# Optimization experiments

Measured on AMD Instinct MI355X. Metric: run time of the kernel, lower is better.

The kernel has to match this reference:

```python
import jax, jax.numpy as jnp
import numpy as np

LEVELS = ((64, 176), (32, 88), (16, 44), (8, 22))
S_TOTAL = sum(h * w for h, w in LEVELS)  # 14960
C = 128; HH = 8; HD = 16; R = 4; L = 4; P = 8
G = 32; PC_MIN = -4.0; PC_MAX = 4.0
NUM_CLASSES = 17; PROP = 3 + 3 + 4 + 1 + NUM_CLASSES  # 28


def _ln(x, g, b):
    m = x.mean(-1, keepdims=True)
    v = ((x - m) ** 2).mean(-1, keepdims=True)
    return (x - m) * jax.lax.rsqrt(v + 1e-5) * g + b


def setup_inputs() -> dict:
    key = jax.random.key(0)
    ks = jax.random.split(key, 20)
    B, N, CAM = 1, 1024, 6
    d = {}
    d['query'] = jax.random.normal(ks[0], (B, N, C), jnp.float32)
    d['gaussian_props'] = jax.random.normal(ks[1], (B, N, PROP), jnp.float32)
    d['ms_feats'] = jax.random.normal(ks[2], (B, CAM, S_TOTAL, C), jnp.float32)
    d['depth_maps'] = jax.random.uniform(ks[3], (B, CAM, 64, 176), jnp.float32, 0.5, 50.0)
    d['lidar2img'] = jax.random.normal(ks[4], (B, CAM, 4, 4), jnp.float32)
    d['img_h'] = 256
    d['img_w'] = 704
    w = lambda k, shp: jax.random.normal(k, shp, jnp.float32) * 0.02
    d['W_sc'] = w(ks[5], (3, 3, 3, C, C)); d['b_sc'] = jnp.zeros((C,), jnp.float32)
    d['sc_g'] = jnp.ones((C,), jnp.float32); d['sc_b'] = jnp.zeros((C,), jnp.float32)
    d['ref_off_w'] = w(ks[6], (C, R * 3)); d['ref_off_b'] = jnp.zeros((R * 3,), jnp.float32)
    d['off_w'] = w(ks[7], (C, HH * R * L * P * 2)); d['off_b'] = jnp.zeros((HH * R * L * P * 2,), jnp.float32)
    d['aw_w'] = w(ks[8], (C, HH * R * L * P)); d['aw_b'] = jnp.zeros((HH * R * L * P,), jnp.float32)
    d['val_w'] = w(ks[9], (C, C)); d['val_b'] = jnp.zeros((C,), jnp.float32)
    d['out_w'] = w(ks[10], (C, C)); d['out_b'] = jnp.zeros((C,), jnp.float32)
    d['an_g'] = jnp.ones((C,), jnp.float32); d['an_b'] = jnp.zeros((C,), jnp.float32)
    d['f1_w'] = w(ks[11], (C, 4 * C)); d['f1_b'] = jnp.zeros((4 * C,), jnp.float32)
    d['f2_w'] = w(ks[12], (4 * C, C)); d['f2_b'] = jnp.zeros((C,), jnp.float32)
    d['fn_g'] = jnp.ones((C,), jnp.float32); d['fn_b'] = jnp.zeros((C,), jnp.float32)
    d['p1_w'] = w(ks[13], (C, C)); d['p1_b'] = jnp.zeros((C,), jnp.float32)
    d['p2_w'] = w(ks[14], (C, PROP)); d['p2_b'] = jnp.zeros((PROP,), jnp.float32)
    return d


def _forward(query, gaussian_props, ms_feats, depth_maps, lidar2img,
             W_sc, b_sc, sc_g, sc_b, ref_off_w, ref_off_b, off_w, off_b,
             aw_w, aw_b, val_w, val_b, out_w, out_b, an_g, an_b,
             f1_w, f1_b, f2_w, f2_b, fn_g, fn_b, p1_w, p1_b, p2_w, p2_b,
             img_h, img_w):
    B, N, _ = query.shape
    CAM = ms_feats.shape[1]
    means = gaussian_props[..., :3]
    # ---- SparseConv3DBlock: scatter-mean voxelization, 3x3x3 conv, gather back ----
    vs = (PC_MAX - PC_MIN) / G
    vox = jnp.clip(jnp.floor((means - PC_MIN) / vs).astype(jnp.int32), 0, G - 1)
    flat = (vox[..., 0] * G + vox[..., 1]) * G + vox[..., 2]  # [B,N]
    bi = jnp.arange(B)[:, None]
    grid = jnp.zeros((B, G * G * G, C), query.dtype).at[bi, flat].add(query)
    cnt = jnp.zeros((B, G * G * G, 1), query.dtype).at[bi, flat].add(1.0)
    grid = (grid / jnp.maximum(cnt, 1.0)).reshape(B, G, G, G, C)
    grid = jax.lax.conv_general_dilated(grid, W_sc, (1, 1, 1), 'SAME',
                                        dimension_numbers=('NDHWC', 'DHWIO', 'NDHWC')) + b_sc
    grid = jax.nn.gelu(grid).reshape(B, G * G * G, C)
    query = _ln(query + grid[bi, flat], sc_g, sc_b)
    # ---- DeformableAttention3D ----
    fW = jnp.asarray(img_w, query.dtype); fH = jnp.asarray(img_h, query.dtype)
    ref3d = means[:, :, None, :] + (query @ ref_off_w + ref_off_b).reshape(B, N, R, 3)
    pts = jnp.concatenate([ref3d, jnp.ones_like(ref3d[..., :1])], -1)
    proj = jnp.einsum('bcij,bnrj->bcnri', lidar2img, pts)  # [B,CAM,N,R,4]
    z = proj[..., 2]; zc = jnp.maximum(z, 1e-5)
    u = proj[..., 0] / zc; v = proj[..., 1] / zc
    valid = (z > 1e-5) & (u >= 0) & (u < fW) & (v >= 0) & (v < fH)
    Hd, Wd = depth_maps.shape[2], depth_maps.shape[3]
    iu = jnp.clip((u / fW * Wd).astype(jnp.int32), 0, Wd - 1)
    iv = jnp.clip((v / fH * Hd).astype(jnp.int32), 0, Hd - 1)
    ds = jnp.take_along_axis(depth_maps.reshape(B, CAM, Hd * Wd),
                             (iv * Wd + iu).reshape(B, CAM, N * R), axis=2).reshape(B, CAM, N, R)
    wmask = jnp.exp(-jnp.abs(z - ds)) * valid.astype(query.dtype)  # [B,CAM,N,R]
    ref2 = jnp.stack([u / fW, v / fH], -1)  # [B,CAM,N,R,2]
    offs = (query @ off_w + off_b).reshape(B, N, HH, R, L, P, 2)
    attn = jax.nn.softmax((query @ aw_w + aw_b).reshape(B, N, HH, R * L * P), -1)
    attn = attn.reshape(B, N, HH, R, L, P)
    value = (ms_feats @ val_w + val_b).reshape(B, CAM, S_TOTAL, HH, HD)
    out = jnp.zeros((B, N, HH, HD), query.dtype)
    s0 = 0
    for l, (Hl, Wl) in enumerate(LEVELS):
        sz = Hl * Wl
        vl = value[:, :, s0:s0 + sz].transpose(0, 1, 3, 2, 4).reshape(B * CAM, HH, sz, HD)
        s0 += sz
        off_l = offs[:, :, :, :, l]  # [B,N,HH,R,P,2]
        loc = ref2[:, :, :, None, :, None, :] + off_l[:, None] / jnp.array([Wl, Hl], query.dtype)
        # loc: [B,CAM,N,HH,R,P,2] in normalized coords
        x = (loc[..., 0] * Wl - 0.5).transpose(0, 1, 3, 2, 4, 5).reshape(B * CAM, HH, N * R * P)
        y = (loc[..., 1] * Hl - 0.5).transpose(0, 1, 3, 2, 4, 5).reshape(B * CAM, HH, N * R * P)
        x0 = jnp.floor(x); y0 = jnp.floor(y); wx = x - x0; wy = y - y0
        x0i = jnp.clip(x0.astype(jnp.int32), 0, Wl - 1)
        x1i = jnp.clip(x0.astype(jnp.int32) + 1, 0, Wl - 1)
        y0i = jnp.clip(y0.astype(jnp.int32), 0, Hl - 1)
        y1i = jnp.clip(y0.astype(jnp.int32) + 1, 0, Hl - 1)
        g = lambda ix, iy: jnp.take_along_axis(vl, (iy * Wl + ix)[..., None], axis=2)
        samp = (((1 - wx) * (1 - wy))[..., None] * g(x0i, y0i)
                + (wx * (1 - wy))[..., None] * g(x1i, y0i)
                + ((1 - wx) * wy)[..., None] * g(x0i, y1i)
                + (wx * wy)[..., None] * g(x1i, y1i))  # [B*CAM,HH,N*R*P,HD]
        samp = samp.reshape(B, CAM, HH, N, R, P, HD)
        ws = attn[:, :, :, :, l, :][:, None].transpose(0, 1, 3, 2, 4, 5) * wmask[:, :, None, :, :, None]
        out = out + jnp.einsum('bchnrp,bchnrpd->bnhd', ws, samp)
    attn_out = out.reshape(B, N, C) @ out_w + out_b
    query = _ln(query + attn_out, an_g, an_b)
    query = _ln(query + (jax.nn.gelu(query @ f1_w + f1_b) @ f2_w + f2_b), fn_g, fn_b)
    props = gaussian_props + (jax.nn.gelu(query @ p1_w + p1_b) @ p2_w + p2_b)
    return query, props


def reference(query, gaussian_props, ms_feats, depth_maps, lidar2img,
              W_sc, b_sc, sc_g, sc_b, ref_off_w, ref_off_b, off_w, off_b,
              aw_w, aw_b, val_w, val_b, out_w, out_b, an_g, an_b,
              f1_w, f1_b, f2_w, f2_b, fn_g, fn_b, p1_w, p1_b, p2_w, p2_b,
              img_h, img_w):
    return _forward(query, gaussian_props, ms_feats, depth_maps, lidar2img,
                    W_sc, b_sc, sc_g, sc_b, ref_off_w, ref_off_b, off_w, off_b,
                    aw_w, aw_b, val_w, val_b, out_w, out_b, an_g, an_b,
                    f1_w, f1_b, f2_w, f2_b, fn_g, fn_b, p1_w, p1_b, p2_w, p2_b,
                    img_h, img_w)
```

## Files before the change

kernel.cpp:

```cpp
#include <hip/hip_runtime.h>
#include <hip/hip_bf16.h>
#include <math.h>

#define NQ    1024
#define CC    128
#define CAM   6
#define RR    4
#define LL    4
#define PP    8
#define HHD   8
#define HDD   16
#define GG    32
#define S_TOT 14960
#define PROPN 28
#define NTAP  27
#define MVAL  (CAM * S_TOT)
#define NVB   ((MVAL + 63) / 64)

typedef __attribute__((ext_vector_type(8))) short bf16x8;
typedef __attribute__((ext_vector_type(4))) float f32x4;

__device__ __forceinline__ float gelu_tanh(float x) {
    return 0.5f * x * (1.0f + tanhf(0.7978845608028654f * (x + 0.044715f * x * x * x)));
}

__device__ __forceinline__ unsigned short f2bf(float f) {
    union { float f; unsigned int u; } x; x.f = f;
    unsigned int r = (x.u + 0x7FFFu + ((x.u >> 16) & 1u)) >> 16;
    return (unsigned short)r;
}

__device__ __forceinline__ float bf2f(short s) {
    union { unsigned int u; float f; } x;
    x.u = ((unsigned int)(unsigned short)s) << 16;
    return x.f;
}

__global__ void k_wt_scatter(const float* __restrict__ Wsc, unsigned short* __restrict__ WscT,
                             const float* __restrict__ valw, unsigned short* __restrict__ valwT,
                             const float* __restrict__ outw, unsigned short* __restrict__ outwT,
                             const float* __restrict__ p1w, unsigned short* __restrict__ p1wT,
                             const float* __restrict__ f1w, unsigned short* __restrict__ f1wT,
                             const float* __restrict__ f2w, unsigned short* __restrict__ f2wT,
                             const float* __restrict__ offw, unsigned short* __restrict__ offwT,
                             const float* __restrict__ aww, unsigned short* __restrict__ awwT,
                             const float* __restrict__ p2w, unsigned short* __restrict__ p2wT,
                             const float* __restrict__ p2b, float* __restrict__ p2bp,
                             const float* __restrict__ qin, const float* __restrict__ gp,
                             float* __restrict__ grid, float* __restrict__ cnt,
                             int* __restrict__ flatidx) {
    __shared__ float t[64][65];
    __shared__ int sflat[2];
    int z = blockIdx.z;
    int tid = threadIdx.x;

    if (z >= 63) {
        int half = tid >> 7, c = tid & 127;
        int n = ((z - 63) * 4 + (blockIdx.x * 2 + blockIdx.y)) * 2 + half;
        if (c == 0) {
            float mx = gp[n * PROPN + 0], my = gp[n * PROPN + 1], mz = gp[n * PROPN + 2];
            int vx = (int)floorf((mx + 4.0f) * 4.0f);
            int vy = (int)floorf((my + 4.0f) * 4.0f);
            int vz = (int)floorf((mz + 4.0f) * 4.0f);
            vx = min(max(vx, 0), GG - 1);
            vy = min(max(vy, 0), GG - 1);
            vz = min(max(vz, 0), GG - 1);
            int f = (vx * GG + vy) * GG + vz;
            sflat[half] = f;
            flatidx[n] = f;
            atomicAdd(&cnt[f], 1.0f);
        }
        __syncthreads();
        atomicAdd(&grid[(size_t)sflat[half] * CC + c], qin[(size_t)n * CC + c]);
        return;
    }

    int n0 = blockIdx.x * 64, k0 = blockIdx.y * 64;
    if (z == 62) {
#pragma unroll
        for (int it = 0; it < 16; ++it) {
            int idx = tid + it * 256;
            int r = idx >> 6, c = idx & 63;
            t[r][c] = (n0 + c < PROPN) ? p2w[(size_t)(k0 + r) * PROPN + n0 + c] : 0.f;
        }
        __syncthreads();
#pragma unroll
        for (int it = 0; it < 16; ++it) {
            int idx = tid + it * 256;
            int r = idx >> 6, c = idx & 63;
            p2wT[(size_t)(n0 + r) * 128 + k0 + c] = f2bf(t[c][r]);
        }
        if (blockIdx.x == 0 && blockIdx.y == 0 && tid < 128)
            p2bp[tid] = (tid < PROPN) ? p2b[tid] : 0.f;
        return;
    }
    const float* src; unsigned short* dst; int ss, ds;
    if (z < 27)       { src = Wsc + (size_t)z * 16384; dst = WscT + (size_t)z * 16384; ss = 128; ds = 128; }
    else if (z == 27) { src = valw; dst = valwT; ss = 128; ds = 128; }
    else if (z == 28) { src = outw; dst = outwT; ss = 128; ds = 128; }
    else if (z == 29) { src = p1w;  dst = p1wT;  ss = 128; ds = 128; }
    else if (z < 34)  { int q = z - 30; src = f1w + q * 128; dst = f1wT + (size_t)q * 16384; ss = 512;  ds = 128; }
    else if (z < 38)  { int q = z - 34; src = f2w + (size_t)q * 16384; dst = f2wT + q * 128; ss = 128;  ds = 512; }
    else if (z < 54)  { int q = z - 38; src = offw + q * 128; dst = offwT + (size_t)q * 16384; ss = 2048; ds = 128; }
    else              { int q = z - 54; src = aww + q * 128;  dst = awwT + (size_t)q * 16384; ss = 1024; ds = 128; }
#pragma unroll
    for (int it = 0; it < 16; ++it) {
        int idx = tid + it * 256;
        int r = idx >> 6, c = idx & 63;
        t[r][c] = src[(size_t)(k0 + r) * ss + n0 + c];
    }
    __syncthreads();
#pragma unroll
    for (int it = 0; it < 16; ++it) {
        int idx = tid + it * 256;
        int r = idx >> 6, c = idx & 63;
        dst[(size_t)(n0 + r) * ds + k0 + c] = f2bf(t[c][r]);
    }
}

__global__ __launch_bounds__(256) void k_conv1m(
    const float* __restrict__ grid, const float* __restrict__ cnt,
    const int* __restrict__ flatidx, const unsigned short* __restrict__ WT,
    float* __restrict__ convacc27) {
    __shared__ bf16x8 As[128 * 16];
    __shared__ bf16x8 Bs[128 * 16];
    __shared__ int   nbase[128];
    __shared__ float nscale[128];
    int tid = threadIdx.x;
    int tap = blockIdx.y;
    int q0 = blockIdx.x * 128;
    int dz = tap / 9 - 1, dy = (tap / 3) % 3 - 1, dx = tap % 3 - 1;

    if (tid < 128) {
        int f = flatidx[q0 + tid];
        int nx = (f >> 10) + dz, ny = ((f >> 5) & 31) + dy, nz = (f & 31) + dx;
        bool ok = (nx >= 0 && nx < GG && ny >= 0 && ny < GG && nz >= 0 && nz < GG);
        int nf = ok ? (nx * GG + ny) * GG + nz : 0;
        nbase[tid] = nf;
        nscale[tid] = ok ? 1.0f / fmaxf(cnt[nf], 1.0f) : 0.f;
    }
    __syncthreads();
#pragma unroll
    for (int it = 0; it < 8; ++it) {
        int idx = tid + it * 256;
        int m = idx >> 4, c = idx & 15;
        const float* p = grid + (size_t)nbase[m] * CC + c * 8;
        float s = nscale[m];
        float4 a = *(const float4*)p;
        float4 b = *(const float4*)(p + 4);
        bf16x8 u;
        u[0] = (short)f2bf(a.x * s); u[1] = (short)f2bf(a.y * s);
        u[2] = (short)f2bf(a.z * s); u[3] = (short)f2bf(a.w * s);
        u[4] = (short)f2bf(b.x * s); u[5] = (short)f2bf(b.y * s);
        u[6] = (short)f2bf(b.z * s); u[7] = (short)f2bf(b.w * s);
        As[m * 16 + (c ^ (m & 15))] = u;
    }
    const unsigned short* Wt = WT + (size_t)tap * CC * CC;
#pragma unroll
    for (int it = 0; it < 8; ++it) {
        int idx = tid + it * 256;
        int n = idx >> 4, c = idx & 15;
        bf16x8 w = *(const bf16x8*)(Wt + (size_t)n * CC + c * 8);
        Bs[n * 16 + (c ^ (n & 15))] = w;
    }
    __syncthreads();

    int lane = tid & 63, wv = tid >> 6;
    int wr = (wv >> 1) * 64, wc = (wv & 1) * 64;
    int r = lane & 15, q = lane >> 4;
    f32x4 acc[4][4];
#pragma unroll
    for (int i = 0; i < 4; ++i)
#pragma unroll
        for (int j = 0; j < 4; ++j)
#pragma unroll
            for (int e = 0; e < 4; ++e) acc[i][j][e] = 0.f;
#pragma unroll
    for (int ks = 0; ks < 4; ++ks) {
        bf16x8 bfr[4];
#pragma unroll
        for (int j = 0; j < 4; ++j)
            bfr[j] = Bs[(wc + j * 16 + r) * 16 + ((ks * 4 + q) ^ r)];
#pragma unroll
        for (int i = 0; i < 4; ++i) {
            bf16x8 af = As[(wr + i * 16 + r) * 16 + ((ks * 4 + q) ^ r)];
#pragma unroll
            for (int j = 0; j < 4; ++j)
                acc[i][j] = __builtin_amdgcn_mfma_f32_16x16x32_bf16(af, bfr[j], acc[i][j], 0, 0, 0);
        }
    }
    float* dst = convacc27 + (size_t)tap * NQ * CC;
#pragma unroll
    for (int i = 0; i < 4; ++i)
#pragma unroll
        for (int e = 0; e < 4; ++e) {
            int m = q0 + wr + i * 16 + q * 4 + e;
#pragma unroll
            for (int j = 0; j < 4; ++j) {
                int col = wc + j * 16 + r;
                dst[(size_t)m * CC + col] = acc[i][j][e];
            }
        }
}

__global__ void k_ln_conv_proj(const float* __restrict__ a, const float* __restrict__ convacc27,
                               const float* __restrict__ bconv,
                               const float* __restrict__ g, const float* __restrict__ be,
                               float* __restrict__ out, unsigned short* __restrict__ outbf,
                               const float* __restrict__ refw, const float* __restrict__ refb,
                               const float* __restrict__ gp, const float* __restrict__ l2i,
                               const float* __restrict__ depth,
                               const int* __restrict__ ih, const int* __restrict__ iw,
                               float* __restrict__ wm, float* __restrict__ r2u,
                               float* __restrict__ r2v) {
    int n = blockIdx.x, c = threadIdx.x;
    float apart = 0.f;
#pragma unroll
    for (int t = 0; t < NTAP; ++t) apart += convacc27[((size_t)t * NQ + n) * CC + c];
    float x = a[n * CC + c] + gelu_tanh(apart + bconv[c]);
    __shared__ float w4[4];
    __shared__ float qrow[CC];
    __shared__ float ro[12];
    float s = x;
#pragma unroll
    for (int d = 1; d < 64; d <<= 1) s += __shfl_xor(s, d);
    if ((c & 63) == 0) w4[c >> 6] = s;
    __syncthreads();
    float m = (w4[0] + w4[1]) * (1.0f / CC);
    float dd = x - m;
    float v = dd * dd;
#pragma unroll
    for (int d = 1; d < 64; d <<= 1) v += __shfl_xor(v, d);
    if ((c & 63) == 0) w4[2 + (c >> 6)] = v;
    __syncthreads();
    float var = (w4[2] + w4[3]) * (1.0f / CC);
    float qv = dd * rsqrtf(var + 1e-5f) * g[c] + be[c];
    out[n * CC + c] = qv;
    outbf[n * CC + c] = f2bf(qv);
    qrow[c] = qv;
    __syncthreads();
    if (c < 12) {
        float sacc = refb[c];
#pragma unroll 4
        for (int k = 0; k < 128; ++k) sacc += qrow[k] * refw[k * 12 + c];
        ro[c] = sacc;
    }
    __syncthreads();
    if (c < 24) {
        int cam = c >> 2, r = c & 3;
        float fH = (float)(*ih), fW = (float)(*iw);
        const float* M = l2i + cam * 16;
        float px = gp[n * PROPN + 0] + ro[r * 3 + 0];
        float py = gp[n * PROPN + 1] + ro[r * 3 + 1];
        float pz = gp[n * PROPN + 2] + ro[r * 3 + 2];
        float p0 = M[0] * px + M[1] * py + M[2]  * pz + M[3];
        float p1 = M[4] * px + M[5] * py + M[6]  * pz + M[7];
        float p2 = M[8] * px + M[9] * py + M[10] * pz + M[11];
        float zc = fmaxf(p2, 1e-5f);
        float u = p0 / zc, vv = p1 / zc;
        bool valid = (p2 > 1e-5f) && (u >= 0.f) && (u < fW) && (vv >= 0.f) && (vv < fH);
        int iu = min(max((int)(u / fW * 176.f), 0), 175);
        int iv = min(max((int)(vv / fH * 64.f), 0), 63);
        float ds = depth[cam * 64 * 176 + iv * 176 + iu];
        int o = cam * (NQ * RR) + n * RR + r;
        wm[o]  = valid ? expf(-fabsf(p2 - ds)) : 0.f;
        r2u[o] = u / fW;
        r2v[o] = vv / fH;
    }
}

union QVSm {
    bf16x8 Bs[128 * 16];
    struct { bf16x8 Bs[128 * 16]; unsigned short Os[64 * 128]; float sbias[128]; } v;
};
__global__ __launch_bounds__(256) void k_qhead_val(
    const unsigned short* __restrict__ Abf,
    const unsigned short* __restrict__ offwT, const float* __restrict__ offb,
    unsigned short* __restrict__ offsb,
    const unsigned short* __restrict__ awwT, const float* __restrict__ awb,
    unsigned short* __restrict__ attn,
    const float* __restrict__ ms, const unsigned short* __restrict__ valwT,
    const float* __restrict__ valb, unsigned short* __restrict__ value)
{
    __shared__ QVSm sm;
    int bx = blockIdx.x, tid = threadIdx.x;
    int lane = tid & 63, wv = tid >> 6;
    int r = lane & 15, q = lane >> 4;

    if (bx >= 24) {
        int vb = (bx - 24) * 8 + blockIdx.y;
        if (vb >= NVB) return;
        int m0 = vb * 64;
#pragma unroll
        for (int it = 0; it < 8; ++it) {
            int idx = tid + it * 256;
            int n = idx >> 4, c = idx & 15;
            sm.v.Bs[n * 16 + (c ^ (n & 15))] = *(const bf16x8*)(valwT + (size_t)n * 128 + c * 8);
        }
        if (tid < 128) sm.v.sbias[tid] = valb[tid];
        __syncthreads();

        int row = m0 + wv * 16 + r;
        int mg = min(row, MVAL - 1);
        const float* pA = ms + (size_t)mg * 128;

        f32x4 acc[8];
#pragma unroll
        for (int j = 0; j < 8; ++j)
#pragma unroll
            for (int e = 0; e < 4; ++e) acc[j][e] = 0.f;

#pragma unroll
        for (int ks = 0; ks < 4; ++ks) {
            const float* p = pA + ks * 32 + q * 8;
            float4 a = *(const float4*)p;
            float4 b = *(const float4*)(p + 4);
            bf16x8 af;
            af[0] = (short)f2bf(a.x); af[1] = (short)f2bf(a.y);
            af[2] = (short)f2bf(a.z); af[3] = (short)f2bf(a.w);
            af[4] = (short)f2bf(b.x); af[5] = (short)f2bf(b.y);
            af[6] = (short)f2bf(b.z); af[7] = (short)f2bf(b.w);
            bf16x8 bfr[8];
#pragma unroll
            for (int j = 0; j < 8; ++j)
                bfr[j] = sm.v.Bs[(j * 16 + r) * 16 + ((ks * 4 + q) ^ r)];
#pragma unroll
            for (int j = 0; j < 8; ++j)
                acc[j] = __builtin_amdgcn_mfma_f32_16x16x32_bf16(af, bfr[j], acc[j], 0, 0, 0);
        }

#pragma unroll
        for (int j = 0; j < 8; ++j)
#pragma unroll
            for (int e = 0; e < 4; ++e) {
                int rl = wv * 16 + q * 4 + e;
                sm.v.Os[rl * 128 + j * 16 + r] = f2bf(acc[j][e] + sm.v.sbias[j * 16 + r]);
            }
        __syncthreads();
#pragma unroll
        for (int it = 0; it < 2; ++it) {
            int idx = tid + it * 256;
            int rl = idx & 63, h = idx >> 6;
            int m = m0 + rl;
            if (m < MVAL) {
                int cam = m / S_TOT;
                int s = m - cam * S_TOT;
                int pos, HW, sb;
                if (s < 11264)      { pos = s;          HW = 11264; sb = 0; }
                else if (s < 14080) { pos = s - 11264;  HW = 2816;  sb = 11264; }
                else if (s < 14784) { pos = s - 14080;  HW = 704;   sb = 14080; }
                else                { pos = s - 14784;  HW = 176;   sb = 14784; }
                size_t dst = ((size_t)cam * S_TOT + sb) * CC
                           + (size_t)h * (HW * HDD) + (size_t)pos * HDD;
                *(bf16x8*)(value + dst)     = *(const bf16x8*)&sm.v.Os[rl * 128 + h * 16];
                *(bf16x8*)(value + dst + 8) = *(const bf16x8*)&sm.v.Os[rl * 128 + h * 16 + 8];
            }
        }
        return;
    }

    bool isoff = bx < 16;
    int n0 = (isoff ? bx : (bx - 16)) * 128;
    const unsigned short* WT = isoff ? offwT : awwT;
    int m0 = blockIdx.y * 128;
    int mw = m0 + wv * 32;

#pragma unroll
    for (int it = 0; it < 8; ++it) {
        int idx = tid + it * 256;
        int n = idx >> 4, c = idx & 15;
        sm.Bs[n * 16 + (c ^ (n & 15))] = *(const bf16x8*)(WT + (size_t)(n0 + n) * 128 + c * 8);
    }
    __syncthreads();

    f32x4 acc[2][8];
#pragma unroll
    for (int i = 0; i < 2; ++i)
#pragma unroll
        for (int j = 0; j < 8; ++j)
#pragma unroll
            for (int e = 0; e < 4; ++e) acc[i][j][e] = 0.f;

#pragma unroll
    for (int ks = 0; ks < 4; ++ks) {
        bf16x8 af[2];
#pragma unroll
        for (int i = 0; i < 2; ++i)
            af[i] = *(const bf16x8*)(Abf + (size_t)(mw + i * 16 + r) * 128 + (ks * 4 + q) * 8);
#pragma unroll
        for (int j = 0; j < 8; ++j) {
            bf16x8 b = sm.Bs[(j * 16 + r) * 16 + ((ks * 4 + q) ^ r)];
#pragma unroll
            for (int i = 0; i < 2; ++i)
                acc[i][j] = __builtin_amdgcn_mfma_f32_16x16x32_bf16(af[i], b, acc[i][j], 0, 0, 0);
        }
    }

    float bia[8];
    const float* bsrc = isoff ? offb : awb;
#pragma unroll
    for (int j = 0; j < 8; ++j) bia[j] = bsrc[n0 + j * 16 + r];

    if (isoff) {
#pragma unroll
        for (int i = 0; i < 2; ++i)
#pragma unroll
            for (int e = 0; e < 4; ++e) {
                int m = mw + i * 16 + q * 4 + e;
                unsigned short* orow = offsb + (size_t)m * 2048 + n0;
#pragma unroll
                for (int j = 0; j < 8; ++j)
                    orow[j * 16 + r] = f2bf(acc[i][j][e] + bia[j]);
            }
    } else {
#pragma unroll
        for (int i = 0; i < 2; ++i)
#pragma unroll
            for (int e = 0; e < 4; ++e) {
                float mx = -1e30f;
#pragma unroll
                for (int j = 0; j < 8; ++j) mx = fmaxf(mx, acc[i][j][e] + bia[j]);
#pragma unroll
                for (int d = 1; d < 16; d <<= 1) mx = fmaxf(mx, __shfl_xor(mx, d));
                float ex[8];
                float sum = 0.f;
#pragma unroll
                for (int j = 0; j < 8; ++j) { ex[j] = expf(acc[i][j][e] + bia[j] - mx); sum += ex[j]; }
#pragma unroll
                for (int d = 1; d < 16; d <<= 1) sum += __shfl_xor(sum, d);
                float inv = 1.0f / sum;
                int m = mw + i * 16 + q * 4 + e;
                unsigned short* orow = attn + (size_t)m * 1024 + n0;
#pragma unroll
                for (int j = 0; j < 8; ++j)
                    orow[j * 16 + r] = f2bf(ex[j] * inv);
            }
    }
}

__global__ __launch_bounds__(512) void k_sample(
                         const unsigned short* __restrict__ value,
                         const unsigned short* __restrict__ offsb,
                         const unsigned short* __restrict__ attn,
                         const float* __restrict__ wm,
// ... 311 lines not shown
        int m = m0 + q * 4 + e;
        int cl = wc + r;
        if (cl < PROPN)
            outp[(size_t)m * PROPN + cl] = acc[e] + p2bp[cl] + gp[(size_t)m * PROPN + cl];
    }
}

extern "C" void kernel_launch(void* const* d_in, const int* in_sizes, int n_in,
                              void* d_out, int out_size, void* d_ws, size_t ws_size,
                              hipStream_t stream) {
    const float* query = (const float*)d_in[0];
    const float* gp    = (const float*)d_in[1];
    const float* ms    = (const float*)d_in[2];
    const float* depth = (const float*)d_in[3];
    const float* l2i   = (const float*)d_in[4];
    const int*   ih    = (const int*)d_in[5];
    const int*   iw    = (const int*)d_in[6];
    const float* Wsc   = (const float*)d_in[7];
    const float* bsc   = (const float*)d_in[8];
    const float* scg   = (const float*)d_in[9];
    const float* scb   = (const float*)d_in[10];
    const float* refw  = (const float*)d_in[11];
    const float* refb  = (const float*)d_in[12];
    const float* offw  = (const float*)d_in[13];
    const float* offbi = (const float*)d_in[14];
    const float* aww   = (const float*)d_in[15];
    const float* awb   = (const float*)d_in[16];
    const float* valw  = (const float*)d_in[17];
    const float* valb  = (const float*)d_in[18];
    const float* outw  = (const float*)d_in[19];
    const float* outb  = (const float*)d_in[20];
    const float* ang   = (const float*)d_in[21];
    const float* anb   = (const float*)d_in[22];
    const float* f1w   = (const float*)d_in[23];
    const float* f1b   = (const float*)d_in[24];
    const float* f2w   = (const float*)d_in[25];
    const float* f2b   = (const float*)d_in[26];
    const float* fng   = (const float*)d_in[27];
    const float* fnb   = (const float*)d_in[28];
    const float* p1w   = (const float*)d_in[29];
    const float* p1b   = (const float*)d_in[30];
    const float* p2w   = (const float*)d_in[31];
    const float* p2b   = (const float*)d_in[32];

    float* outq = (float*)d_out;
    float* outp = outq + NQ * CC;

    float* ws = (float*)d_ws;
    size_t o = 0;
    float* grid    = ws + o; o += (size_t)GG * GG * GG * CC;
    float* cnt     = ws + o; o += GG * GG * GG;
    size_t zero_floats = o;
    int*   flatidx = (int*)(ws + o); o += NQ;
    float* convacc27 = ws + o; o += (size_t)NTAP * NQ * CC;
    float* q1      = ws + o; o += NQ * CC;
    float* wm      = ws + o; o += CAM * NQ * RR;
    float* r2u     = ws + o; o += CAM * NQ * RR;
    float* r2v     = ws + o; o += CAM * NQ * RR;
    float* sampout = ws + o; o += NQ * CC;
    float* p2bp    = ws + o; o += 128;
    unsigned short* u16base = (unsigned short*)(ws + o);
    size_t uo = 0;
    unsigned short* value = u16base + uo; uo += (size_t)CAM * S_TOT * CC;
    unsigned short* offsb = u16base + uo; uo += (size_t)NQ * 2048;
    unsigned short* attn  = u16base + uo; uo += (size_t)NQ * 1024;
    unsigned short* q1bf  = u16base + uo; uo += (size_t)NQ * CC;
    unsigned short* offwT = u16base + uo; uo += (size_t)2048 * 128;
    unsigned short* awwT  = u16base + uo; uo += (size_t)1024 * 128;
    unsigned short* valwT = u16base + uo; uo += 128 * 128;
    unsigned short* outwT = u16base + uo; uo += 128 * 128;
    unsigned short* f1wT  = u16base + uo; uo += 512 * 128;
    unsigned short* f2wT  = u16base + uo; uo += 128 * 512;
    unsigned short* p1wT  = u16base + uo; uo += 128 * 128;
    unsigned short* p2wT  = u16base + uo; uo += 128 * 128;
    unsigned short* WscT  = u16base + uo; uo += (size_t)27 * 128 * 128;
    (void)ws_size; (void)in_sizes; (void)n_in; (void)out_size;

    hipMemsetAsync(ws, 0, zero_floats * sizeof(float), stream);

    k_wt_scatter<<<dim3(2, 2, 63 + 128), 256, 0, stream>>>(
        Wsc, WscT, valw, valwT, outw, outwT, p1w, p1wT, f1w, f1wT, f2w, f2wT,
        offw, offwT, aww, awwT, p2w, p2wT, p2b, p2bp,
        query, gp, grid, cnt, flatidx);

    k_conv1m<<<dim3(8, 27), 256, 0, stream>>>(grid, cnt, flatidx, WscT, convacc27);
    k_ln_conv_proj<<<NQ, CC, 0, stream>>>(query, convacc27, bsc, scg, scb, q1, q1bf,
                                          refw, refb, gp, l2i, depth, ih, iw, wm, r2u, r2v);

    k_qhead_val<<<dim3(24 + 176, 8), 256, 0, stream>>>(
        q1bf, offwT, offbi, offsb, awwT, awb, attn,
        ms, valwT, valb, value);

    k_sample<<<NQ, 512, 0, stream>>>(value, offsb, attn, wm, r2u, r2v, sampout);

    k_tail<<<64, 512, 0, stream>>>(sampout, outwT, outb, q1, ang, anb,
                                   f1wT, f1b, f2wT, f2b, fng, fnb,
                                   p1wT, p1b, p2wT, p2bp, gp, outq, outp);
}
```

Before: 221.5 us.

## Fuse sparse-conv tap loop with LayerNorm/projection and co-schedule with value projection

The 27-tap sparse conv now accumulates all taps in registers within one block per 128 queries, instead of writing 27 partial tiles to global memory and reducing them in a separate kernel. The GELU, LayerNorm, reference-offset projection and camera projection run in the same kernel epilogue. That kernel also hosts the value-projection blocks, so the value GEMM overlaps with the serial conv blocks. The query-head GEMM becomes its own launch. This removes the large convacc27 buffer traffic and one launch, but only 8 blocks now handle the conv, each looping serially over 27 taps, which limits parallelism on that path.

```diff
diff --git a/kernel.cpp b/kernel.cpp
--- a/kernel.cpp
+++ b/kernel.cpp
@@ -34,6 +34,15 @@
     union { unsigned int u; float f; } x;
     x.u = ((unsigned int)(unsigned short)s) << 16;
     return x.f;
+}
+
+__device__ __forceinline__ void nbns_calc(int f, int tap, const float* __restrict__ cnt,
+                                          int& nfo, float& nso) {
+    int dz = tap / 9 - 1, dy = (tap / 3) % 3 - 1, dx = tap % 3 - 1;
+    int nx = (f >> 10) + dz, ny = ((f >> 5) & 31) + dy, nz = (f & 31) + dx;
+    bool ok = (nx >= 0 && nx < GG && ny >= 0 && ny < GG && nz >= 0 && nz < GG);
+    nfo = ok ? (nx * GG + ny) * GG + nz : 0;
+    nso = ok ? 1.0f / fmaxf(cnt[nfo], 1.0f) : 0.f;
 }
 
 __global__ void k_wt_scatter(const float* __restrict__ Wsc, unsigned short* __restrict__ WscT,
@@ -118,178 +127,35 @@
     }
 }
 
-__global__ __launch_bounds__(256) void k_conv1m(
+union CLSm {
+    struct { bf16x8 As[128 * 16]; bf16x8 Bs[128 * 16]; } c;
+    float xrow[128 * 128];
+    struct { bf16x8 Bs[128 * 16]; unsigned short Os[64 * 128]; float sbias[128]; } v;
+};
+__global__ __launch_bounds__(256) void k_conv_ln_val(
     const float* __restrict__ grid, const float* __restrict__ cnt,
     const int* __restrict__ flatidx, const unsigned short* __restrict__ WT,
-    float* __restrict__ convacc27) {
-    __shared__ bf16x8 As[128 * 16];
-    __shared__ bf16x8 Bs[128 * 16];
-    __shared__ int   nbase[128];
-    __shared__ float nscale[128];
-    int tid = threadIdx.x;
-    int tap = blockIdx.y;
-    int q0 = blockIdx.x * 128;
-    int dz = tap / 9 - 1, dy = (tap / 3) % 3 - 1, dx = tap % 3 - 1;
-
-    if (tid < 128) {
-        int f = flatidx[q0 + tid];
-        int nx = (f >> 10) + dz, ny = ((f >> 5) & 31) + dy, nz = (f & 31) + dx;
-        bool ok = (nx >= 0 && nx < GG && ny >= 0 && ny < GG && nz >= 0 && nz < GG);
-        int nf = ok ? (nx * GG + ny) * GG + nz : 0;
-        nbase[tid] = nf;
-        nscale[tid] = ok ? 1.0f / fmaxf(cnt[nf], 1.0f) : 0.f;
-    }
-    __syncthreads();
-#pragma unroll
-    for (int it = 0; it < 8; ++it) {
-        int idx = tid + it * 256;
-        int m = idx >> 4, c = idx & 15;
-        const float* p = grid + (size_t)nbase[m] * CC + c * 8;
-        float s = nscale[m];
-        float4 a = *(const float4*)p;
-        float4 b = *(const float4*)(p + 4);
-        bf16x8 u;
-        u[0] = (short)f2bf(a.x * s); u[1] = (short)f2bf(a.y * s);
-        u[2] = (short)f2bf(a.z * s); u[3] = (short)f2bf(a.w * s);
-        u[4] = (short)f2bf(b.x * s); u[5] = (short)f2bf(b.y * s);
-        u[6] = (short)f2bf(b.z * s); u[7] = (short)f2bf(b.w * s);
-        As[m * 16 + (c ^ (m & 15))] = u;
-    }
-    const unsigned short* Wt = WT + (size_t)tap * CC * CC;
-#pragma unroll
-    for (int it = 0; it < 8; ++it) {
-        int idx = tid + it * 256;
-        int n = idx >> 4, c = idx & 15;
-        bf16x8 w = *(const bf16x8*)(Wt + (size_t)n * CC + c * 8);
-        Bs[n * 16 + (c ^ (n & 15))] = w;
-    }
-    __syncthreads();
-
-    int lane = tid & 63, wv = tid >> 6;
-    int wr = (wv >> 1) * 64, wc = (wv & 1) * 64;
-    int r = lane & 15, q = lane >> 4;
-    f32x4 acc[4][4];
-#pragma unroll
-    for (int i = 0; i < 4; ++i)
-#pragma unroll
-        for (int j = 0; j < 4; ++j)
-#pragma unroll
-            for (int e = 0; e < 4; ++e) acc[i][j][e] = 0.f;
-#pragma unroll
-    for (int ks = 0; ks < 4; ++ks) {
-        bf16x8 bfr[4];
-#pragma unroll
-        for (int j = 0; j < 4; ++j)
-            bfr[j] = Bs[(wc + j * 16 + r) * 16 + ((ks * 4 + q) ^ r)];
-#pragma unroll
-        for (int i = 0; i < 4; ++i) {
-            bf16x8 af = As[(wr + i * 16 + r) * 16 + ((ks * 4 + q) ^ r)];
-#pragma unroll
-            for (int j = 0; j < 4; ++j)
-                acc[i][j] = __builtin_amdgcn_mfma_f32_16x16x32_bf16(af, bfr[j], acc[i][j], 0, 0, 0);
-        }
-    }
-    float* dst = convacc27 + (size_t)tap * NQ * CC;
-#pragma unroll
-    for (int i = 0; i < 4; ++i)
-#pragma unroll
-        for (int e = 0; e < 4; ++e) {
-            int m = q0 + wr + i * 16 + q * 4 + e;
-#pragma unroll
-            for (int j = 0; j < 4; ++j) {
-                int col = wc + j * 16 + r;
-                dst[(size_t)m * CC + col] = acc[i][j][e];
-            }
-        }
-}
-
-__global__ void k_ln_conv_proj(const float* __restrict__ a, const float* __restrict__ convacc27,
-                               const float* __restrict__ bconv,
-                               const float* __restrict__ g, const float* __restrict__ be,
-                               float* __restrict__ out, unsigned short* __restrict__ outbf,
-                               const float* __restrict__ refw, const float* __restrict__ refb,
-                               const float* __restrict__ gp, const float* __restrict__ l2i,
-                               const float* __restrict__ depth,
-                               const int* __restrict__ ih, const int* __restrict__ iw,
-                               float* __restrict__ wm, float* __restrict__ r2u,
-                               float* __restrict__ r2v) {
-    int n = blockIdx.x, c = threadIdx.x;
-    float apart = 0.f;
-#pragma unroll
-    for (int t = 0; t < NTAP; ++t) apart += convacc27[((size_t)t * NQ + n) * CC + c];
-    float x = a[n * CC + c] + gelu_tanh(apart + bconv[c]);
-    __shared__ float w4[4];
-    __shared__ float qrow[CC];
-    __shared__ float ro[12];
-    float s = x;
-#pragma unroll
-    for (int d = 1; d < 64; d <<= 1) s += __shfl_xor(s, d);
-    if ((c & 63) == 0) w4[c >> 6] = s;
-    __syncthreads();
-    float m = (w4[0] + w4[1]) * (1.0f / CC);
-    float dd = x - m;
-    float v = dd * dd;
-#pragma unroll
-    for (int d = 1; d < 64; d <<= 1) v += __shfl_xor(v, d);
-    if ((c & 63) == 0) w4[2 + (c >> 6)] = v;
-    __syncthreads();
-    float var = (w4[2] + w4[3]) * (1.0f / CC);
-    float qv = dd * rsqrtf(var + 1e-5f) * g[c] + be[c];
-    out[n * CC + c] = qv;
-    outbf[n * CC + c] = f2bf(qv);
-    qrow[c] = qv;
-    __syncthreads();
-    if (c < 12) {
-        float sacc = refb[c];
-#pragma unroll 4
-        for (int k = 0; k < 128; ++k) sacc += qrow[k] * refw[k * 12 + c];
-        ro[c] = sacc;
-    }
-    __syncthreads();
-    if (c < 24) {
-        int cam = c >> 2, r = c & 3;
-        float fH = (float)(*ih), fW = (float)(*iw);
-        const float* M = l2i + cam * 16;
-        float px = gp[n * PROPN + 0] + ro[r * 3 + 0];
-        float py = gp[n * PROPN + 1] + ro[r * 3 + 1];
-        float pz = gp[n * PROPN + 2] + ro[r * 3 + 2];
-        float p0 = M[0] * px + M[1] * py + M[2]  * pz + M[3];
-        float p1 = M[4] * px + M[5] * py + M[6]  * pz + M[7];
-        float p2 = M[8] * px + M[9] * py + M[10] * pz + M[11];
-        float zc = fmaxf(p2, 1e-5f);
-        float u = p0 / zc, vv = p1 / zc;
-        bool valid = (p2 > 1e-5f) && (u >= 0.f) && (u < fW) && (vv >= 0.f) && (vv < fH);
-        int iu = min(max((int)(u / fW * 176.f), 0), 175);
-        int iv = min(max((int)(vv / fH * 64.f), 0), 63);
-        float ds = depth[cam * 64 * 176 + iv * 176 + iu];
-        int o = cam * (NQ * RR) + n * RR + r;
-        wm[o]  = valid ? expf(-fabsf(p2 - ds)) : 0.f;
-        r2u[o] = u / fW;
-        r2v[o] = vv / fH;
-    }
-}
-
-union QVSm {
-    bf16x8 Bs[128 * 16];
-    struct { bf16x8 Bs[128 * 16]; unsigned short Os[64 * 128]; float sbias[128]; } v;
-};
-__global__ __launch_bounds__(256) void k_qhead_val(
-    const unsigned short* __restrict__ Abf,
-    const unsigned short* __restrict__ offwT, const float* __restrict__ offb,
-    unsigned short* __restrict__ offsb,
-    const unsigned short* __restrict__ awwT, const float* __restrict__ awb,
-    unsigned short* __restrict__ attn,
+    const float* __restrict__ a, const float* __restrict__ bconv,
+    const float* __restrict__ g, const float* __restrict__ be,
+    float* __restrict__ q1, unsigned short* __restrict__ q1bf,
+    const float* __restrict__ refw, const float* __restrict__ refb,
+    const float* __restrict__ gp, const float* __restrict__ l2i,
+    const float* __restrict__ depth,
+    const int* __restrict__ ih, const int* __restrict__ iw,
+    float* __restrict__ wm, float* __restrict__ r2u, float* __restrict__ r2v,
     const float* __restrict__ ms, const unsigned short* __restrict__ valwT,
     const float* __restrict__ valb, unsigned short* __restrict__ value)
 {
-    __shared__ QVSm sm;
+    __shared__ CLSm sm;
+    __shared__ int   nb[128];
+    __shared__ float ns[128];
+    __shared__ float roAll[128 * 12];
     int bx = blockIdx.x, tid = threadIdx.x;
     int lane = tid & 63, wv = tid >> 6;
     int r = lane & 15, q = lane >> 4;
 
-    if (bx >= 24) {
-        int vb = (bx - 24) * 8 + blockIdx.y;
-        if (vb >= NVB) return;
+    if (bx >= 8) {
+        int vb = bx - 8;
         int m0 = vb * 64;
 #pragma unroll
         for (int it = 0; it < 8; ++it) {
@@ -313,13 +179,13 @@
 #pragma unroll
         for (int ks = 0; ks < 4; ++ks) {
             const float* p = pA + ks * 32 + q * 8;
-            float4 a = *(const float4*)p;
-            float4 b = *(const float4*)(p + 4);
+            float4 aa = *(const float4*)p;
+            float4 bb = *(const float4*)(p + 4);
             bf16x8 af;
-            af[0] = (short)f2bf(a.x); af[1] = (short)f2bf(a.y);
-            af[2] = (short)f2bf(a.z); af[3] = (short)f2bf(a.w);
-            af[4] = (short)f2bf(b.x); af[5] = (short)f2bf(b.y);
-            af[6] = (short)f2bf(b.z); af[7] = (short)f2bf(b.w);
+            af[0] = (short)f2bf(aa.x); af[1] = (short)f2bf(aa.y);
+            af[2] = (short)f2bf(aa.z); af[3] = (short)f2bf(aa.w);
+            af[4] = (short)f2bf(bb.x); af[5] = (short)f2bf(bb.y);
+            af[6] = (short)f2bf(bb.z); af[7] = (short)f2bf(bb.w);
             bf16x8 bfr[8];
 #pragma unroll
             for (int j = 0; j < 8; ++j)
@@ -359,6 +225,163 @@
         return;
     }
 
+    int q0 = bx * 128;
+    int wr = (wv >> 1) * 64, wc = (wv & 1) * 64;
+    int myflat = (tid < 128) ? flatidx[q0 + tid] : 0;
+    if (tid < 128) {
+        int nfo; float nso;
+        nbns_calc(myflat, 0, cnt, nfo, nso);
+        nb[tid] = nfo; ns[tid] = nso;
+    }
+    __syncthreads();
+
+    f32x4 acc[4][4];
+#pragma unroll
+    for (int i = 0; i < 4; ++i)
+#pragma unroll
+        for (int j = 0; j < 4; ++j)
+#pragma unroll
+            for (int e = 0; e < 4; ++e) acc[i][j][e] = 0.f;
+
+    for (int tap = 0; tap < NTAP; ++tap) {
+#pragma unroll
+        for (int it = 0; it < 8; ++it) {
+            int idx = tid + it * 256;
+            int m = idx >> 4, c = idx & 15;
+            const float* p = grid + (size_t)nb[m] * CC + c * 8;
+            float s = ns[m];
+            float4 aa = *(const float4*)p;
+            float4 bb = *(const float4*)(p + 4);
+            bf16x8 u;
+            u[0] = (short)f2bf(aa.x * s); u[1] = (short)f2bf(aa.y * s);
+            u[2] = (short)f2bf(aa.z * s); u[3] = (short)f2bf(aa.w * s);
+            u[4] = (short)f2bf(bb.x * s); u[5] = (short)f2bf(bb.y * s);
+            u[6] = (short)f2bf(bb.z * s); u[7] = (short)f2bf(bb.w * s);
+            sm.c.As[m * 16 + (c ^ (m & 15))] = u;
+        }
+        const unsigned short* Wt = WT + (size_t)tap * CC * CC;
+#pragma unroll
+        for (int it = 0; it < 8; ++it) {
+            int idx = tid + it * 256;
+            int n = idx >> 4, c = idx & 15;
+            sm.c.Bs[n * 16 + (c ^ (n & 15))] = *(const bf16x8*)(Wt + (size_t)n * CC + c * 8);
+        }
+        __syncthreads();
+        if (tid < 128 && tap < NTAP - 1) {
+            int nfo; float nso;
+            nbns_calc(myflat, tap + 1, cnt, nfo, nso);
+            nb[tid] = nfo; ns[tid] = nso;
+        }
+#pragma unroll
+        for (int ks = 0; ks < 4; ++ks) {
+            bf16x8 bfr[4];
+#pragma unroll
+            for (int j = 0; j < 4; ++j)
+                bfr[j] = sm.c.Bs[(wc + j * 16 + r) * 16 + ((ks * 4 + q) ^ r)];
+#pragma unroll
+            for (int i = 0; i < 4; ++i) {
+                bf16x8 af = sm.c.As[(wr + i * 16 + r) * 16 + ((ks * 4 + q) ^ r)];
+#pragma unroll
+                for (int j = 0; j < 4; ++j)
+                    acc[i][j] = __builtin_amdgcn_mfma_f32_16x16x32_bf16(af, bfr[j], acc[i][j], 0, 0, 0);
+            }
+        }
+        __syncthreads();
+    }
+
+#pragma unroll
+    for (int i = 0; i < 4; ++i)
+#pragma unroll
+        for (int e = 0; e < 4; ++e) {
+            int row = wr + i * 16 + q * 4 + e;
+            int n = q0 + row;
+#pragma unroll
+            for (int j = 0; j < 4; ++j) {
+                int col = wc + j * 16 + r;
+                float x = a[(size_t)n * CC + col] + gelu_tanh(acc[i][j][e] + bconv[col]);
+                sm.xrow[row * 128 + col] = x;
+            }
+        }
+    __syncthreads();
+
+    {
+        float g0 = g[lane], g1 = g[lane + 64];
+        float b0 = be[lane], b1 = be[lane + 64];
+        for (int i = 0; i < 32; ++i) {
+            int row = wv * 32 + i;
+            float x0 = sm.xrow[row * 128 + lane];
+            float x1 = sm.xrow[row * 128 + lane + 64];
+            float s = x0 + x1;
+#pragma unroll
+            for (int d = 1; d < 64; d <<= 1) s += __shfl_xor(s, d);
+            float mean = s * (1.0f / 128.0f);
+            float d0 = x0 - mean, d1 = x1 - mean;
+            float v = d0 * d0 + d1 * d1;
+#pragma unroll
+            for (int d = 1; d < 64; d <<= 1) v += __shfl_xor(v, d);
+            float rstd = rsqrtf(v * (1.0f / 128.0f) + 1e-5f);
+            float qv0 = d0 * rstd * g0 + b0;
+            float qv1 = d1 * rstd * g1 + b1;
+            int n = q0 + row;
+            q1[(size_t)n * CC + lane]      = qv0;
+            q1[(size_t)n * CC + lane + 64] = qv1;
+            q1bf[(size_t)n * CC + lane]      = f2bf(qv0);
+            q1bf[(size_t)n * CC + lane + 64] = f2bf(qv1);
+            sm.xrow[row * 128 + lane]      = qv0;
+            sm.xrow[row * 128 + lane + 64] = qv1;
+        }
+    }
+    __syncthreads();
+
+#pragma unroll
+    for (int j = 0; j < 6; ++j) {
+        int d = tid + j * 256;
+        int qq = d / 12, cc = d - qq * 12;
+        float sacc = refb[cc];
+#pragma unroll 4
+        for (int k = 0; k < 128; ++k) sacc += sm.xrow[qq * 128 + k] * refw[k * 12 + cc];
+        roAll[qq * 12 + cc] = sacc;
+    }
+    __syncthreads();
+
+    float fH = (float)(*ih), fW = (float)(*iw);
+#pragma unroll
+    for (int j = 0; j < 12; ++j) {
+        int item = tid + j * 256;
+        int nl = item / 24, c24 = item - nl * 24;
+        int cam = c24 >> 2, rr = c24 & 3;
+        const float* M = l2i + cam * 16;
+        int n = q0 + nl;
+        float px = gp[n * PROPN + 0] + roAll[nl * 12 + rr * 3 + 0];
+        float py = gp[n * PROPN + 1] + roAll[nl * 12 + rr * 3 + 1];
+        float pz = gp[n * PROPN + 2] + roAll[nl * 12 + rr * 3 + 2];
+        float p0 = M[0] * px + M[1] * py + M[2]  * pz + M[3];
+        float p1 = M[4] * px + M[5] * py + M[6]  * pz + M[7];
+        float p2 = M[8] * px + M[9] * py + M[10] * pz + M[11];
+        float zc = fmaxf(p2, 1e-5f);
+        float u = p0 / zc, vv = p1 / zc;
+        bool valid = (p2 > 1e-5f) && (u >= 0.f) && (u < fW) && (vv >= 0.f) && (vv < fH);
+        int iu = min(max((int)(u / fW * 176.f), 0), 175);
+        int iv = min(max((int)(vv / fH * 64.f), 0), 63);
+        float ds = depth[cam * 64 * 176 + iv * 176 + iu];
+        int o = cam * (NQ * RR) + n * RR + rr;
+        wm[o]  = valid ? expf(-fabsf(p2 - ds)) : 0.f;
+        r2u[o] = u / fW;
+        r2v[o] = vv / fH;
+    }
+}
+
+__global__ __launch_bounds__(256) void k_qhead(
+    const unsigned short* __restrict__ Abf,
+    const unsigned short* __restrict__ offwT, const float* __restrict__ offb,
+    unsigned short* __restrict__ offsb,
+    const unsigned short* __restrict__ awwT, const float* __restrict__ awb,
+    unsigned short* __restrict__ attn)
+{
+    __shared__ bf16x8 Bs[128 * 16];
+    int bx = blockIdx.x, tid = threadIdx.x;
+    int lane = tid & 63, wv = tid >> 6;
+    int r = lane & 15, q = lane >> 4;
     bool isoff = bx < 16;
     int n0 = (isoff ? bx : (bx - 16)) * 128;
     const unsigned short* WT = isoff ? offwT : awwT;
@@ -369,7 +392,7 @@
     for (int it = 0; it < 8; ++it) {
         int idx = tid + it * 256;
         int n = idx >> 4, c = idx & 15;
-        sm.Bs[n * 16 + (c ^ (n & 15))] = *(const bf16x8*)(WT + (size_t)(n0 + n) * 128 + c * 8);
+        Bs[n * 16 + (c ^ (n & 15))] = *(const bf16x8*)(WT + (size_t)(n0 + n) * 128 + c * 8);
     }
     __syncthreads();
 
@@ -389,7 +412,7 @@
             af[i] = *(const bf16x8*)(Abf + (size_t)(mw + i * 16 + r) * 128 + (ks * 4 + q) * 8);
 #pragma unroll
         for (int j = 0; j < 8; ++j) {
-            bf16x8 b = sm.Bs[(j * 16 + r) * 16 + ((ks * 4 + q) ^ r)];
+            bf16x8 b = Bs[(j * 16 + r) * 16 + ((ks * 4 + q) ^ r)];
 #pragma unroll
             for (int i = 0; i < 2; ++i)
                 acc[i][j] = __builtin_amdgcn_mfma_f32_16x16x32_bf16(af[i], b, acc[i][j], 0, 0, 0);
@@ -807,7 +830,6 @@
     float* cnt     = ws + o; o += GG * GG * GG;
     size_t zero_floats = o;
     int*   flatidx = (int*)(ws + o); o += NQ;
-    float* convacc27 = ws + o; o += (size_t)NTAP * NQ * CC;
     float* q1      = ws + o; o += NQ * CC;
     float* wm      = ws + o; o += CAM * NQ * RR;
     float* r2u     = ws + o; o += CAM * NQ * RR;
@@ -838,13 +860,13 @@
         offw, offwT, aww, awwT, p2w, p2wT, p2b, p2bp,
         query, gp, grid, cnt, flatidx);
 
-    k_conv1m<<<dim3(8, 27), 256, 0, stream>>>(grid, cnt, flatidx, WscT, convacc27);
-    k_ln_conv_proj<<<NQ, CC, 0, stream>>>(query, convacc27, bsc, scg, scb, q1, q1bf,
-                                          refw, refb, gp, l2i, depth, ih, iw, wm, r2u, r2v);
-
-    k_qhead_val<<<dim3(24 + 176, 8), 256, 0, stream>>>(
-        q1bf, offwT, offbi, offsb, awwT, awb, attn,
+    k_conv_ln_val<<<dim3(8 + NVB), 256, 0, stream>>>(
+        grid, cnt, flatidx, WscT,
+        query, bsc, scg, scb, q1, q1bf,
+        refw, refb, gp, l2i, depth, ih, iw, wm, r2u, r2v,
         ms, valwT, valb, value);
+
+    k_qhead<<<dim3(24, 8), 256, 0, stream>>>(q1bf, offwT, offbi, offsb, awwT, awb, attn);
 
     k_sample<<<NQ, 512, 0, stream>>>(value, offsb, attn, wm, r2u, r2v, sampout);
 
```

Measured after the change: 494.0 us. 123% more time.

## Move value projection into the conv kernel launch to overlap with conv

Applied to the files above, without the earlier changes.

The value projection blocks (ms_feats times val_w, scattered into a per-head layout) move out of the query-head kernel and into the submanifold conv kernel as extra blocks of the same grid. This lets the large, bandwidth-bound value GEMM run alongside the small 27-tap conv, which on its own launches only 216 blocks. The query-head kernel then only computes offsets and attention weights. The shared-memory union grows to cover both the conv A/B tiles and the value staging buffers, which may lower occupancy for the value blocks.

```diff
diff --git a/kernel.cpp b/kernel.cpp
--- a/kernel.cpp
+++ b/kernel.cpp
@@ -16,6 +16,7 @@
 #define NTAP  27
 #define MVAL  (CAM * S_TOT)
 #define NVB   ((MVAL + 63) / 64)
+#define NCVB  (8 * NTAP)
 
 typedef __attribute__((ext_vector_type(8))) short bf16x8;
 typedef __attribute__((ext_vector_type(4))) float f32x4;
@@ -118,17 +119,97 @@
     }
 }
 
-__global__ __launch_bounds__(256) void k_conv1m(
+union CVSm {
+    struct { bf16x8 As[128 * 16]; bf16x8 Bs[128 * 16]; } c;
+    struct { bf16x8 Bs[128 * 16]; unsigned short Os[64 * 128]; float sbias[128]; } v;
+};
+__global__ __launch_bounds__(256) void k_conv_val(
     const float* __restrict__ grid, const float* __restrict__ cnt,
     const int* __restrict__ flatidx, const unsigned short* __restrict__ WT,
-    float* __restrict__ convacc27) {
-    __shared__ bf16x8 As[128 * 16];
-    __shared__ bf16x8 Bs[128 * 16];
+    float* __restrict__ convacc27,
+    const float* __restrict__ ms, const unsigned short* __restrict__ valwT,
+    const float* __restrict__ valb, unsigned short* __restrict__ value)
+{
+    __shared__ CVSm sm;
     __shared__ int   nbase[128];
     __shared__ float nscale[128];
-    int tid = threadIdx.x;
-    int tap = blockIdx.y;
-    int q0 = blockIdx.x * 128;
+    int bx = blockIdx.x, tid = threadIdx.x;
+    int lane = tid & 63, wv = tid >> 6;
+    int r = lane & 15, q = lane >> 4;
+
+    if (bx >= NCVB) {
+        int vb = bx - NCVB;
+        int m0 = vb * 64;
+#pragma unroll
+        for (int it = 0; it < 8; ++it) {
+            int idx = tid + it * 256;
+            int n = idx >> 4, c = idx & 15;
+            sm.v.Bs[n * 16 + (c ^ (n & 15))] = *(const bf16x8*)(valwT + (size_t)n * 128 + c * 8);
+        }
+        if (tid < 128) sm.v.sbias[tid] = valb[tid];
+        __syncthreads();
+
+        int row = m0 + wv * 16 + r;
+        int mg = min(row, MVAL - 1);
+        const float* pA = ms + (size_t)mg * 128;
+
+        f32x4 acc[8];
+#pragma unroll
+        for (int j = 0; j < 8; ++j)
+#pragma unroll
+            for (int e = 0; e < 4; ++e) acc[j][e] = 0.f;
+
+#pragma unroll
+        for (int ks = 0; ks < 4; ++ks) {
+            const float* p = pA + ks * 32 + q * 8;
+            float4 aa = *(const float4*)p;
+            float4 bb = *(const float4*)(p + 4);
+            bf16x8 af;
+            af[0] = (short)f2bf(aa.x); af[1] = (short)f2bf(aa.y);
+            af[2] = (short)f2bf(aa.z); af[3] = (short)f2bf(aa.w);
+            af[4] = (short)f2bf(bb.x); af[5] = (short)f2bf(bb.y);
+            af[6] = (short)f2bf(bb.z); af[7] = (short)f2bf(bb.w);
+            bf16x8 bfr[8];
+#pragma unroll
+            for (int j = 0; j < 8; ++j)
+                bfr[j] = sm.v.Bs[(j * 16 + r) * 16 + ((ks * 4 + q) ^ r)];
+#pragma unroll
+            for (int j = 0; j < 8; ++j)
+                acc[j] = __builtin_amdgcn_mfma_f32_16x16x32_bf16(af, bfr[j], acc[j], 0, 0, 0);
+        }
+
+#pragma unroll
+        for (int j = 0; j < 8; ++j)
+#pragma unroll
+            for (int e = 0; e < 4; ++e) {
+                int rl = wv * 16 + q * 4 + e;
+                sm.v.Os[rl * 128 + j * 16 + r] = f2bf(acc[j][e] + sm.v.sbias[j * 16 + r]);
+            }
+        __syncthreads();
+#pragma unroll
+        for (int it = 0; it < 2; ++it) {
+            int idx = tid + it * 256;
+            int rl = idx & 63, h = idx >> 6;
+            int m = m0 + rl;
+            if (m < MVAL) {
+                int cam = m / S_TOT;
+                int s = m - cam * S_TOT;
+                int pos, HW, sb;
+                if (s < 11264)      { pos = s;          HW = 11264; sb = 0; }
+                else if (s < 14080) { pos = s - 11264;  HW = 2816;  sb = 11264; }
+                else if (s < 14784) { pos = s - 14080;  HW = 704;   sb = 14080; }
+                else                { pos = s - 14784;  HW = 176;   sb = 14784; }
+                size_t dst = ((size_t)cam * S_TOT + sb) * CC
+                           + (size_t)h * (HW * HDD) + (size_t)pos * HDD;
+                *(bf16x8*)(value + dst)     = *(const bf16x8*)&sm.v.Os[rl * 128 + h * 16];
+                *(bf16x8*)(value + dst + 8) = *(const bf16x8*)&sm.v.Os[rl * 128 + h * 16 + 8];
+            }
+        }
+        return;
+    }
+
+    int tap = bx >> 3;
+    int q0 = (bx & 7) * 128;
     int dz = tap / 9 - 1, dy = (tap / 3) % 3 - 1, dx = tap % 3 - 1;
 
     if (tid < 128) {
@@ -153,7 +234,7 @@
         u[2] = (short)f2bf(a.z * s); u[3] = (short)f2bf(a.w * s);
         u[4] = (short)f2bf(b.x * s); u[5] = (short)f2bf(b.y * s);
         u[6] = (short)f2bf(b.z * s); u[7] = (short)f2bf(b.w * s);
-        As[m * 16 + (c ^ (m & 15))] = u;
+        sm.c.As[m * 16 + (c ^ (m & 15))] = u;
     }
     const unsigned short* Wt = WT + (size_t)tap * CC * CC;
 #pragma unroll
@@ -161,13 +242,11 @@
         int idx = tid + it * 256;
         int n = idx >> 4, c = idx & 15;
         bf16x8 w = *(const bf16x8*)(Wt + (size_t)n * CC + c * 8);
-        Bs[n * 16 + (c ^ (n & 15))] = w;
-    }
-    __syncthreads();
-
-    int lane = tid & 63, wv = tid >> 6;
+        sm.c.Bs[n * 16 + (c ^ (n & 15))] = w;
+    }
+    __syncthreads();
+
     int wr = (wv >> 1) * 64, wc = (wv & 1) * 64;
-    int r = lane & 15, q = lane >> 4;
     f32x4 acc[4][4];
 #pragma unroll
     for (int i = 0; i < 4; ++i)
@@ -180,10 +259,10 @@
         bf16x8 bfr[4];
 #pragma unroll
         for (int j = 0; j < 4; ++j)
-            bfr[j] = Bs[(wc + j * 16 + r) * 16 + ((ks * 4 + q) ^ r)];
+            bfr[j] = sm.c.Bs[(wc + j * 16 + r) * 16 + ((ks * 4 + q) ^ r)];
 #pragma unroll
         for (int i = 0; i < 4; ++i) {
-            bf16x8 af = As[(wr + i * 16 + r) * 16 + ((ks * 4 + q) ^ r)];
+            bf16x8 af = sm.c.As[(wr + i * 16 + r) * 16 + ((ks * 4 + q) ^ r)];
 #pragma unroll
             for (int j = 0; j < 4; ++j)
                 acc[i][j] = __builtin_amdgcn_mfma_f32_16x16x32_bf16(af, bfr[j], acc[i][j], 0, 0, 0);
@@ -269,96 +348,17 @@
     }
 }
 
-union QVSm {
-    bf16x8 Bs[128 * 16];
-    struct { bf16x8 Bs[128 * 16]; unsigned short Os[64 * 128]; float sbias[128]; } v;
-};
-__global__ __launch_bounds__(256) void k_qhead_val(
+__global__ __launch_bounds__(256) void k_qhead(
     const unsigned short* __restrict__ Abf,
     const unsigned short* __restrict__ offwT, const float* __restrict__ offb,
     unsigned short* __restrict__ offsb,
     const unsigned short* __restrict__ awwT, const float* __restrict__ awb,
-    unsigned short* __restrict__ attn,
-    const float* __restrict__ ms, const unsigned short* __restrict__ valwT,
-    const float* __restrict__ valb, unsigned short* __restrict__ value)
+    unsigned short* __restrict__ attn)
 {
-    __shared__ QVSm sm;
+    __shared__ bf16x8 Bs[128 * 16];
     int bx = blockIdx.x, tid = threadIdx.x;
     int lane = tid & 63, wv = tid >> 6;
     int r = lane & 15, q = lane >> 4;
-
-    if (bx >= 24) {
-        int vb = (bx - 24) * 8 + blockIdx.y;
-        if (vb >= NVB) return;
-        int m0 = vb * 64;
-#pragma unroll
-        for (int it = 0; it < 8; ++it) {
-            int idx = tid + it * 256;
-            int n = idx >> 4, c = idx & 15;
-            sm.v.Bs[n * 16 + (c ^ (n & 15))] = *(const bf16x8*)(valwT + (size_t)n * 128 + c * 8);
-        }
-        if (tid < 128) sm.v.sbias[tid] = valb[tid];
-        __syncthreads();
-
-        int row = m0 + wv * 16 + r;
-        int mg = min(row, MVAL - 1);
-        const float* pA = ms + (size_t)mg * 128;
-
-        f32x4 acc[8];
-#pragma unroll
-        for (int j = 0; j < 8; ++j)
-#pragma unroll
-            for (int e = 0; e < 4; ++e) acc[j][e] = 0.f;
-
-#pragma unroll
-        for (int ks = 0; ks < 4; ++ks) {
-            const float* p = pA + ks * 32 + q * 8;
-            float4 a = *(const float4*)p;
-            float4 b = *(const float4*)(p + 4);
-            bf16x8 af;
-            af[0] = (short)f2bf(a.x); af[1] = (short)f2bf(a.y);
-            af[2] = (short)f2bf(a.z); af[3] = (short)f2bf(a.w);
-            af[4] = (short)f2bf(b.x); af[5] = (short)f2bf(b.y);
-            af[6] = (short)f2bf(b.z); af[7] = (short)f2bf(b.w);
-            bf16x8 bfr[8];
-#pragma unroll
-            for (int j = 0; j < 8; ++j)
-                bfr[j] = sm.v.Bs[(j * 16 + r) * 16 + ((ks * 4 + q) ^ r)];
-#pragma unroll
-            for (int j = 0; j < 8; ++j)
-                acc[j] = __builtin_amdgcn_mfma_f32_16x16x32_bf16(af, bfr[j], acc[j], 0, 0, 0);
-        }
-
-#pragma unroll
-        for (int j = 0; j < 8; ++j)
-#pragma unroll
-            for (int e = 0; e < 4; ++e) {
-                int rl = wv * 16 + q * 4 + e;
-                sm.v.Os[rl * 128 + j * 16 + r] = f2bf(acc[j][e] + sm.v.sbias[j * 16 + r]);
-            }
-        __syncthreads();
-#pragma unroll
-        for (int it = 0; it < 2; ++it) {
-            int idx = tid + it * 256;
-            int rl = idx & 63, h = idx >> 6;
-            int m = m0 + rl;
-            if (m < MVAL) {
-                int cam = m / S_TOT;
-                int s = m - cam * S_TOT;
-                int pos, HW, sb;
-                if (s < 11264)      { pos = s;          HW = 11264; sb = 0; }
-                else if (s < 14080) { pos = s - 11264;  HW = 2816;  sb = 11264; }
-                else if (s < 14784) { pos = s - 14080;  HW = 704;   sb = 14080; }
-                else                { pos = s - 14784;  HW = 176;   sb = 14784; }
-                size_t dst = ((size_t)cam * S_TOT + sb) * CC
-                           + (size_t)h * (HW * HDD) + (size_t)pos * HDD;
-                *(bf16x8*)(value + dst)     = *(const bf16x8*)&sm.v.Os[rl * 128 + h * 16];
-                *(bf16x8*)(value + dst + 8) = *(const bf16x8*)&sm.v.Os[rl * 128 + h * 16 + 8];
-            }
-        }
-        return;
-    }
-
     bool isoff = bx < 16;
     int n0 = (isoff ? bx : (bx - 16)) * 128;
     const unsigned short* WT = isoff ? offwT : awwT;
@@ -369,7 +369,7 @@
     for (int it = 0; it < 8; ++it) {
         int idx = tid + it * 256;
         int n = idx >> 4, c = idx & 15;
-        sm.Bs[n * 16 + (c ^ (n & 15))] = *(const bf16x8*)(WT + (size_t)(n0 + n) * 128 + c * 8);
+        Bs[n * 16 + (c ^ (n & 15))] = *(const bf16x8*)(WT + (size_t)(n0 + n) * 128 + c * 8);
     }
     __syncthreads();
 
@@ -389,7 +389,7 @@
             af[i] = *(const bf16x8*)(Abf + (size_t)(mw + i * 16 + r) * 128 + (ks * 4 + q) * 8);
 #pragma unroll
         for (int j = 0; j < 8; ++j) {
-            bf16x8 b = sm.Bs[(j * 16 + r) * 16 + ((ks * 4 + q) ^ r)];
+            bf16x8 b = Bs[(j * 16 + r) * 16 + ((ks * 4 + q) ^ r)];
 #pragma unroll
             for (int i = 0; i < 2; ++i)
                 acc[i][j] = __builtin_amdgcn_mfma_f32_16x16x32_bf16(af[i], b, acc[i][j], 0, 0, 0);
@@ -838,13 +838,14 @@
         offw, offwT, aww, awwT, p2w, p2wT, p2b, p2bp,
         query, gp, grid, cnt, flatidx);
 
-    k_conv1m<<<dim3(8, 27), 256, 0, stream>>>(grid, cnt, flatidx, WscT, convacc27);
+    k_conv_val<<<dim3(NCVB + NVB), 256, 0, stream>>>(
+        grid, cnt, flatidx, WscT, convacc27,
+        ms, valwT, valb, value);
+
     k_ln_conv_proj<<<NQ, CC, 0, stream>>>(query, convacc27, bsc, scg, scb, q1, q1bf,
                                           refw, refb, gp, l2i, depth, ih, iw, wm, r2u, r2v);
 
-    k_qhead_val<<<dim3(24 + 176, 8), 256, 0, stream>>>(
-        q1bf, offwT, offbi, offsb, awwT, awb, attn,
-        ms, valwT, valb, value);
+    k_qhead<<<dim3(24, 8), 256, 0, stream>>>(q1bf, offwT, offbi, offsb, awwT, awb, attn);
 
     k_sample<<<NQ, 512, 0, stream>>>(value, offsb, attn, wm, r2u, r2v, sampout);
 
```

Measured after the change: 221.4 us. About the same (-0.0%).
